# Performance work log

Hardware: AMD Instinct MI355X
Metric: run time of the kernel (lower is better)

The kernel has to match this reference:

```python
import jax, jax.numpy as jnp
import numpy as np

VOCAB = 32000
DIM = 1024
SEQ = 4096


def setup_inputs() -> dict:
    key = jax.random.key(0)
    ks = jax.random.split(key, 6)
    x = jax.random.randint(ks[0], (1, SEQ), 0, VOCAB, dtype=jnp.int64 if jax.config.jax_enable_x64 else jnp.int32)
    emb = jax.random.normal(ks[1], (VOCAB, DIM), dtype=jnp.float32) * 0.02
    norm_w = jnp.ones((DIM,), dtype=jnp.float32)
    Wq = jax.random.normal(ks[2], (DIM, DIM), dtype=jnp.float32) * (1.0 / np.sqrt(DIM))
    Wk = jax.random.normal(ks[3], (DIM, DIM), dtype=jnp.float32) * (1.0 / np.sqrt(DIM))
    Wv = jax.random.normal(ks[4], (DIM, DIM), dtype=jnp.float32) * (1.0 / np.sqrt(DIM))
    return {"x": x, "emb": emb, "norm_w": norm_w, "Wq": Wq, "Wk": Wk, "Wv": Wv}


def reference(x, emb, norm_w, Wq, Wk, Wv):
    # embedding lookup: [1, S, D]
    h = emb[x]
    # RMSNorm (torch nn.RMSNorm with eps=None -> finfo(dtype).eps)
    eps = jnp.finfo(h.dtype).eps
    h = h * jax.lax.rsqrt(jnp.mean(h * h, axis=-1, keepdims=True) + eps) * norm_w
    h = h[0]  # squeeze(0) -> [S, D]
    # QKV projections (torch Linear: y = x @ W.T)
    q = h @ Wq.T
    k = h @ Wk.T
    v = h @ Wv.T
    # NOTE: faithful to source -- no 1/sqrt(d) scaling, no causal mask
    attn = jax.nn.softmax(q @ k.T, axis=-1)  # [S, S]
    out = attn @ v  # [S, D]
    return jax.nn.silu(out)
```

## Files before the change

kernel.cpp:

```cpp
#include <hip/hip_runtime.h>
#include <stdint.h>

#define SEQ 4096
#define DIM 1024

typedef __bf16 bf16x8 __attribute__((ext_vector_type(8)));
typedef float f32x4 __attribute__((ext_vector_type(4)));
typedef unsigned short u16;

__device__ __forceinline__ u16 f2bf(float f) {
    unsigned u = __float_as_uint(f);
    u += 0x7fffu + ((u >> 16) & 1u);
    return (u16)(u >> 16);
}
__device__ __forceinline__ float bf2f(u16 h) {
    return __uint_as_float(((unsigned)h) << 16);
}

__device__ __forceinline__ void gload16(const u16* g, u16* l) {
    __builtin_amdgcn_global_load_lds(
        (const __attribute__((address_space(1))) void*)g,
        (__attribute__((address_space(3))) void*)l, 16, 0, 0);
}

__global__ __launch_bounds__(256) void embed_rmsnorm_split(
    const int* __restrict__ x, const float* __restrict__ emb,
    const float* __restrict__ nw, u16* __restrict__ hh, u16* __restrict__ hl)
{
    const int row  = blockIdx.x;
    const int t    = threadIdx.x;
    const int lane = t & 63, wave = t >> 6;

    bool i64 = true;
    #pragma unroll
    for (int i = 1; i < 128; i += 2) i64 = i64 && (x[i] == 0);
    const int id = i64 ? x[2 * row] : x[row];

    float4 e = *(const float4*)(emb + (size_t)id * DIM + t * 4);
    float ss = e.x*e.x + e.y*e.y + e.z*e.z + e.w*e.w;
    #pragma unroll
    for (int off = 32; off > 0; off >>= 1) ss += __shfl_down(ss, off);

    __shared__ float red[4];
    if (lane == 0) red[wave] = ss;
    __syncthreads();
    float sum = red[0] + red[1] + red[2] + red[3];
    float scale = rsqrtf(sum * (1.0f / DIM) + 1.1920929e-7f);

    float4 n = *(const float4*)(nw + t * 4);
    float o0 = e.x * scale * n.x;
    float o1 = e.y * scale * n.y;
    float o2 = e.z * scale * n.z;
    float o3 = e.w * scale * n.w;
    ushort4 oh, ol;
    u16 b;
    b = f2bf(o0); oh.x = b; ol.x = f2bf(o0 - bf2f(b));
    b = f2bf(o1); oh.y = b; ol.y = f2bf(o1 - bf2f(b));
    b = f2bf(o2); oh.z = b; ol.z = f2bf(o2 - bf2f(b));
    b = f2bf(o3); oh.w = b; ol.w = f2bf(o3 - bf2f(b));
    *(ushort4*)(hh + (size_t)row * DIM + t * 4) = oh;
    *(ushort4*)(hl + (size_t)row * DIM + t * 4) = ol;
}

__global__ __launch_bounds__(256) void split_w(
    const float* __restrict__ W0, const float* __restrict__ W1,
    const float* __restrict__ W2, u16* __restrict__ H, u16* __restrict__ L)
{
    const float* W = (blockIdx.y == 0) ? W0 : (blockIdx.y == 1) ? W1 : W2;
    const size_t base = (size_t)blockIdx.y * DIM * DIM;
    const int i = (blockIdx.x * 256 + threadIdx.x) * 4;
    float4 w = *(const float4*)(W + i);
    ushort4 h, l;
    u16 b;
    b = f2bf(w.x); h.x = b; l.x = f2bf(w.x - bf2f(b));
    b = f2bf(w.y); h.y = b; l.y = f2bf(w.y - bf2f(b));
    b = f2bf(w.z); h.z = b; l.z = f2bf(w.z - bf2f(b));
    b = f2bf(w.w); h.w = b; l.w = f2bf(w.w - bf2f(b));
    *(ushort4*)(H + base + i) = h;
    *(ushort4*)(L + base + i) = l;
}

template<int OUT_MODE>
__global__ __launch_bounds__(256, 2) void gemm_split3(
    const u16* __restrict__ Ah, const u16* __restrict__ Al, int lda,
    const u16* __restrict__ Bh, const u16* __restrict__ Bl, int ldb,
    void* __restrict__ C0, void* __restrict__ C1, int ldc, int K)
{
    __shared__ __align__(16) u16 Ash[128 * 32];
    __shared__ __align__(16) u16 Asl[128 * 32];
    __shared__ __align__(16) u16 Bsh[128 * 32];
    __shared__ __align__(16) u16 Bsl[128 * 32];

    const int tid  = threadIdx.x;
    const int lane = tid & 63;
    const int wave = tid >> 6;
    const int m0   = blockIdx.y * 128;
    const int n0   = blockIdx.x * 128;
    const int wr   = (wave >> 1) * 64;
    const int wc   = (wave & 1) * 64;
    const int half = lane >> 4;
    const int l16  = lane & 15;

    f32x4 acc[4][4] = {};

    const int arow = tid >> 2;
    const int acol = (tid & 3) * 8;
    const int wb   = wave * 512;

    for (int k0 = 0; k0 < K; k0 += 32) {
        __syncthreads();
        const size_t aoff = (size_t)(m0 + arow) * lda + k0 + acol;
        const size_t boff = (size_t)(n0 + arow) * ldb + k0 + acol;
        gload16(Ah + aoff,                    &Ash[wb]);
        gload16(Ah + aoff + (size_t)64 * lda, &Ash[2048 + wb]);
        gload16(Al + aoff,                    &Asl[wb]);
        gload16(Al + aoff + (size_t)64 * lda, &Asl[2048 + wb]);
        gload16(Bh + boff,                    &Bsh[wb]);
        gload16(Bh + boff + (size_t)64 * ldb, &Bsh[2048 + wb]);
        gload16(Bl + boff,                    &Bsl[wb]);
        gload16(Bl + boff + (size_t)64 * ldb, &Bsl[2048 + wb]);
        __syncthreads();

        bf16x8 afh[4], afl[4], bfh[4], bfl[4];
        #pragma unroll
        for (int i = 0; i < 4; ++i) {
            afh[i] = *(const bf16x8*)&Ash[(wr + i*16 + l16) * 32 + half * 8];
            afl[i] = *(const bf16x8*)&Asl[(wr + i*16 + l16) * 32 + half * 8];
        }
        #pragma unroll
        for (int j = 0; j < 4; ++j) {
            bfh[j] = *(const bf16x8*)&Bsh[(wc + j*16 + l16) * 32 + half * 8];
            bfl[j] = *(const bf16x8*)&Bsl[(wc + j*16 + l16) * 32 + half * 8];
        }
        #pragma unroll
        for (int i = 0; i < 4; ++i)
            #pragma unroll
            for (int j = 0; j < 4; ++j) {
                acc[i][j] = __builtin_amdgcn_mfma_f32_16x16x32_bf16(afh[i], bfh[j], acc[i][j], 0, 0, 0);
                acc[i][j] = __builtin_amdgcn_mfma_f32_16x16x32_bf16(afh[i], bfl[j], acc[i][j], 0, 0, 0);
                acc[i][j] = __builtin_amdgcn_mfma_f32_16x16x32_bf16(afl[i], bfh[j], acc[i][j], 0, 0, 0);
            }
    }

    #pragma unroll
    for (int i = 0; i < 4; ++i)
        #pragma unroll
        for (int j = 0; j < 4; ++j)
            #pragma unroll
            for (int r = 0; r < 4; ++r) {
                int row = m0 + wr + i * 16 + half * 4 + r;
                int col = n0 + wc + j * 16 + l16;
                float val = acc[i][j][r];
                if constexpr (OUT_MODE == 0) {
                    ((float*)C0)[(size_t)row * ldc + col] = val;
                } else if constexpr (OUT_MODE == 1) {
                    u16 hi = f2bf(val);
                    ((u16*)C0)[(size_t)row * ldc + col] = hi;
                    ((u16*)C1)[(size_t)row * ldc + col] = f2bf(val - bf2f(hi));
                } else {
                    ((u16*)C0)[(size_t)col * ldc + row] = f2bf(val);
                }
            }
}

__global__ __launch_bounds__(256, 2) void gemm_bt_silu(
    const u16* __restrict__ A, int lda,
    const u16* __restrict__ B, int ldb,
    float* __restrict__ C, int ldc, int K)
{
    __shared__ __align__(16) u16 As[128 * 32];
    __shared__ __align__(16) u16 Bs[128 * 32];

    const int tid  = threadIdx.x;
    const int lane = tid & 63;
    const int wave = tid >> 6;
    const int m0   = blockIdx.y * 128;
    const int n0   = blockIdx.x * 128;
    const int wr   = (wave >> 1) * 64;
    const int wc   = (wave & 1) * 64;
    const int half = lane >> 4;
    const int l16  = lane & 15;

    f32x4 acc[4][4] = {};
    const int arow = tid >> 2;
    const int acol = (tid & 3) * 8;
    const int wb   = wave * 512;

    for (int k0 = 0; k0 < K; k0 += 32) {
        __syncthreads();
        gload16(A + (size_t)(m0 + arow)      * lda + k0 + acol, &As[wb]);
        gload16(A + (size_t)(m0 + 64 + arow) * lda + k0 + acol, &As[2048 + wb]);
        gload16(B + (size_t)(n0 + arow)      * ldb + k0 + acol, &Bs[wb]);
        gload16(B + (size_t)(n0 + 64 + arow) * ldb + k0 + acol, &Bs[2048 + wb]);
        __syncthreads();

        bf16x8 af[4], bfr[4];
        #pragma unroll
        for (int i = 0; i < 4; ++i)
            af[i] = *(const bf16x8*)&As[(wr + i*16 + l16) * 32 + half * 8];
        #pragma unroll
        for (int j = 0; j < 4; ++j)
            bfr[j] = *(const bf16x8*)&Bs[(wc + j*16 + l16) * 32 + half * 8];
        #pragma unroll
        for (int i = 0; i < 4; ++i)
            #pragma unroll
            for (int j = 0; j < 4; ++j)
                acc[i][j] = __builtin_amdgcn_mfma_f32_16x16x32_bf16(af[i], bfr[j], acc[i][j], 0, 0, 0);
    }

    #pragma unroll
    for (int i = 0; i < 4; ++i)
        #pragma unroll
        for (int j = 0; j < 4; ++j)
            #pragma unroll
            for (int r = 0; r < 4; ++r) {
                int row = m0 + wr + i * 16 + half * 4 + r;
                int col = n0 + wc + j * 16 + l16;
                float v = acc[i][j][r];
                v = v / (1.0f + __expf(-v));
                C[(size_t)row * ldc + col] = v;
            }
}

__global__ __launch_bounds__(256) void softmax_rows(float* __restrict__ S)
{
    const int row  = blockIdx.x;
    const int t    = threadIdx.x;
    const int lane = t & 63, wave = t >> 6;
    float* rp = S + (size_t)row * SEQ;

    float v[16];
    #pragma unroll
    for (int i = 0; i < 4; ++i) {
        float4 f = *(const float4*)(rp + i * 1024 + t * 4);
        v[i*4+0] = f.x; v[i*4+1] = f.y; v[i*4+2] = f.z; v[i*4+3] = f.w;
    }

    float m = v[0];
    #pragma unroll
    for (int i = 1; i < 16; ++i) m = fmaxf(m, v[i]);
    #pragma unroll
    for (int off = 32; off > 0; off >>= 1) m = fmaxf(m, __shfl_down(m, off));
    __shared__ float red[4];
    if (lane == 0) red[wave] = m;
    __syncthreads();
    m = fmaxf(fmaxf(red[0], red[1]), fmaxf(red[2], red[3]));
    __syncthreads();

    float s = 0.0f;
    #pragma unroll
    for (int i = 0; i < 16; ++i) { v[i] = __expf(v[i] - m); s += v[i]; }
    #pragma unroll
    for (int off = 32; off > 0; off >>= 1) s += __shfl_down(s, off);
    if (lane == 0) red[wave] = s;
    __syncthreads();
    s = red[0] + red[1] + red[2] + red[3];
    float inv = 1.0f / s;

    u16* op = (u16*)rp;
    #pragma unroll
    for (int i = 0; i < 4; ++i) {
        ushort4 o;
        o.x = f2bf(v[i*4+0] * inv);
        o.y = f2bf(v[i*4+1] * inv);
        o.z = f2bf(v[i*4+2] * inv);
        o.w = f2bf(v[i*4+3] * inv);
        *(ushort4*)(op + i * 1024 + t * 4) = o;
    }
}

extern "C" void kernel_launch(void* const* d_in, const int* in_sizes, int n_in,
                              void* d_out, int out_size, void* d_ws, size_t ws_size,
                              hipStream_t stream)
{
    const int*   x   = (const int*)d_in[0];
    const float* emb = (const float*)d_in[1];
    const float* nw  = (const float*)d_in[2];
    const float* Wq  = (const float*)d_in[3];
    const float* Wk  = (const float*)d_in[4];
    const float* Wv  = (const float*)d_in[5];
    float* out = (float*)d_out;

    char* ws = (char*)d_ws;
    u16*   vT = (u16*)(ws);
    u16*   qh = (u16*)(ws + ( 8u << 20));
    u16*   ql = (u16*)(ws + (16u << 20));
    u16*   kh = (u16*)(ws + (24u << 20));
    u16*   kl = (u16*)(ws + (32u << 20));
    float* Sc = (float*)(ws + (40u << 20));
    u16*   hh = (u16*)(ws + (40u << 20));
    u16*   hl = (u16*)(ws + (48u << 20));
    u16*   Wh = (u16*)(ws + (56u << 20));
    u16*   Wl = (u16*)(ws + (62u << 20));

    embed_rmsnorm_split<<<SEQ, 256, 0, stream>>>(x, emb, nw, hh, hl);
    split_w<<<dim3(DIM * DIM / 1024, 3), 256, 0, stream>>>(Wq, Wk, Wv, Wh, Wl);

    const size_t WSZ = (size_t)DIM * DIM;
    dim3 gqkv(DIM / 128, SEQ / 128);
    gemm_split3<1><<<gqkv, 256, 0, stream>>>(hh, hl, DIM, Wh,           Wl,           DIM, qh, ql,      DIM, DIM);
    gemm_split3<1><<<gqkv, 256, 0, stream>>>(hh, hl, DIM, Wh + WSZ,     Wl + WSZ,     DIM, kh, kl,      DIM, DIM);
    gemm_split3<2><<<gqkv, 256, 0, stream>>>(hh, hl, DIM, Wh + 2 * WSZ, Wl + 2 * WSZ, DIM, vT, nullptr, SEQ, DIM);

    dim3 gs(SEQ / 128, SEQ / 128);
    gemm_split3<0><<<gs, 256, 0, stream>>>(qh, ql, DIM, kh, kl, DIM, Sc, nullptr, SEQ, DIM);

    softmax_rows<<<SEQ, 256, 0, stream>>>(Sc);

    dim3 gpv(DIM / 128, SEQ / 128);
    gemm_bt_silu<<<gpv, 256, 0, stream>>>((const u16*)Sc, 2 * SEQ, vT, SEQ, out, DIM, SEQ);
}
```

Measured before the change: 535.4 us.

## Fuse QKV GEMMs, concatenate split-bf16 K dim for scores, split-K PV

Merges the three QKV projection launches into one grid over 3072 output columns. Q and K hi/lo halves are stored interleaved so the score GEMM becomes a single bf16 GEMM over a 3072-long K dimension instead of a three-MFMA split loop. The PV GEMM is split along K into two partial results, giving twice as many blocks to fill the GPU, and a separate elementwise kernel sums the partials and applies SiLU. In exchange it adds extra traffic for the partial buffers and one more launch, and raises the occupancy hint to 3 blocks per CU.

```diff
diff --git a/kernel.cpp b/kernel.cpp
--- a/kernel.cpp
+++ b/kernel.cpp
@@ -80,11 +80,10 @@
     *(ushort4*)(L + base + i) = l;
 }
 
-template<int OUT_MODE>
-__global__ __launch_bounds__(256, 2) void gemm_split3(
-    const u16* __restrict__ Ah, const u16* __restrict__ Al, int lda,
-    const u16* __restrict__ Bh, const u16* __restrict__ Bl, int ldb,
-    void* __restrict__ C0, void* __restrict__ C1, int ldc, int K)
+__global__ __launch_bounds__(256, 3) void gemm_qkv(
+    const u16* __restrict__ Ah, const u16* __restrict__ Al,
+    const u16* __restrict__ Bh, const u16* __restrict__ Bl,
+    u16* __restrict__ qhl, u16* __restrict__ khl, u16* __restrict__ vT)
 {
     __shared__ __align__(16) u16 Ash[128 * 32];
     __shared__ __align__(16) u16 Asl[128 * 32];
@@ -107,18 +106,18 @@
     const int acol = (tid & 3) * 8;
     const int wb   = wave * 512;
 
-    for (int k0 = 0; k0 < K; k0 += 32) {
-        __syncthreads();
-        const size_t aoff = (size_t)(m0 + arow) * lda + k0 + acol;
-        const size_t boff = (size_t)(n0 + arow) * ldb + k0 + acol;
-        gload16(Ah + aoff,                    &Ash[wb]);
-        gload16(Ah + aoff + (size_t)64 * lda, &Ash[2048 + wb]);
-        gload16(Al + aoff,                    &Asl[wb]);
-        gload16(Al + aoff + (size_t)64 * lda, &Asl[2048 + wb]);
-        gload16(Bh + boff,                    &Bsh[wb]);
-        gload16(Bh + boff + (size_t)64 * ldb, &Bsh[2048 + wb]);
-        gload16(Bl + boff,                    &Bsl[wb]);
-        gload16(Bl + boff + (size_t)64 * ldb, &Bsl[2048 + wb]);
+    for (int k0 = 0; k0 < DIM; k0 += 32) {
+        __syncthreads();
+        const size_t aoff = (size_t)(m0 + arow) * DIM + k0 + acol;
+        const size_t boff = (size_t)(n0 + arow) * DIM + k0 + acol;
+        gload16(Ah + aoff,            &Ash[wb]);
+        gload16(Ah + aoff + 64 * DIM, &Ash[2048 + wb]);
+        gload16(Al + aoff,            &Asl[wb]);
+        gload16(Al + aoff + 64 * DIM, &Asl[2048 + wb]);
+        gload16(Bh + boff,            &Bsh[wb]);
+        gload16(Bh + boff + 64 * DIM, &Bsh[2048 + wb]);
+        gload16(Bl + boff,            &Bsl[wb]);
+        gload16(Bl + boff + 64 * DIM, &Bsl[2048 + wb]);
         __syncthreads();
 
         bf16x8 afh[4], afl[4], bfh[4], bfl[4];
@@ -142,6 +141,7 @@
             }
     }
 
+    const int reg = n0 >> 10;
     #pragma unroll
     for (int i = 0; i < 4; ++i)
         #pragma unroll
@@ -151,22 +151,23 @@
                 int row = m0 + wr + i * 16 + half * 4 + r;
                 int col = n0 + wc + j * 16 + l16;
                 float val = acc[i][j][r];
-                if constexpr (OUT_MODE == 0) {
-                    ((float*)C0)[(size_t)row * ldc + col] = val;
-                } else if constexpr (OUT_MODE == 1) {
-                    u16 hi = f2bf(val);
-                    ((u16*)C0)[(size_t)row * ldc + col] = hi;
-                    ((u16*)C1)[(size_t)row * ldc + col] = f2bf(val - bf2f(hi));
+                u16 hi = f2bf(val);
+                if (reg == 0) {
+                    qhl[(size_t)row * 2048 + col]        = hi;
+                    qhl[(size_t)row * 2048 + col + 1024] = f2bf(val - bf2f(hi));
+                } else if (reg == 1) {
+                    int c = col - 1024;
+                    khl[(size_t)row * 2048 + c]          = hi;
+                    khl[(size_t)row * 2048 + c + 1024]   = f2bf(val - bf2f(hi));
                 } else {
-                    ((u16*)C0)[(size_t)col * ldc + row] = f2bf(val);
+                    vT[(size_t)(col - 2048) * SEQ + row] = hi;
                 }
             }
 }
 
-__global__ __launch_bounds__(256, 2) void gemm_bt_silu(
-    const u16* __restrict__ A, int lda,
-    const u16* __restrict__ B, int ldb,
-    float* __restrict__ C, int ldc, int K)
+__global__ __launch_bounds__(256, 3) void gemm_sc(
+    const u16* __restrict__ Q, const u16* __restrict__ Kk,
+    float* __restrict__ C)
 {
     __shared__ __align__(16) u16 As[128 * 32];
     __shared__ __align__(16) u16 Bs[128 * 32];
@@ -186,12 +187,14 @@
     const int acol = (tid & 3) * 8;
     const int wb   = wave * 512;
 
-    for (int k0 = 0; k0 < K; k0 += 32) {
-        __syncthreads();
-        gload16(A + (size_t)(m0 + arow)      * lda + k0 + acol, &As[wb]);
-        gload16(A + (size_t)(m0 + 64 + arow) * lda + k0 + acol, &As[2048 + wb]);
-        gload16(B + (size_t)(n0 + arow)      * ldb + k0 + acol, &Bs[wb]);
-        gload16(B + (size_t)(n0 + 64 + arow) * ldb + k0 + acol, &Bs[2048 + wb]);
+    for (int k0 = 0; k0 < 3072; k0 += 32) {
+        const int ka = (k0 < 2048) ? k0 : k0 - 2048;
+        const int kb = (k0 < 1024) ? k0 : k0 - 1024;
+        __syncthreads();
+        gload16(Q  + (size_t)(m0 + arow)      * 2048 + ka + acol, &As[wb]);
+        gload16(Q  + (size_t)(m0 + 64 + arow) * 2048 + ka + acol, &As[2048 + wb]);
+        gload16(Kk + (size_t)(n0 + arow)      * 2048 + kb + acol, &Bs[wb]);
+        gload16(Kk + (size_t)(n0 + 64 + arow) * 2048 + kb + acol, &Bs[2048 + wb]);
         __syncthreads();
 
         bf16x8 af[4], bfr[4];
@@ -216,9 +219,7 @@
             for (int r = 0; r < 4; ++r) {
                 int row = m0 + wr + i * 16 + half * 4 + r;
                 int col = n0 + wc + j * 16 + l16;
-                float v = acc[i][j][r];
-                v = v / (1.0f + __expf(-v));
-                C[(size_t)row * ldc + col] = v;
+                C[(size_t)row * SEQ + col] = acc[i][j][r];
             }
 }
 
@@ -269,6 +270,81 @@
     }
 }
 
+__global__ __launch_bounds__(256, 3) void gemm_pv_partial(
+    const u16* __restrict__ A, const u16* __restrict__ B,
+    float* __restrict__ P0, float* __restrict__ P1)
+{
+    __shared__ __align__(16) u16 As[128 * 32];
+    __shared__ __align__(16) u16 Bs[128 * 32];
+
+    const int tid  = threadIdx.x;
+    const int lane = tid & 63;
+    const int wave = tid >> 6;
+    const int m0   = blockIdx.y * 128;
+    const int n0   = blockIdx.x * 128;
+    const int wr   = (wave >> 1) * 64;
+    const int wc   = (wave & 1) * 64;
+    const int half = lane >> 4;
+    const int l16  = lane & 15;
+
+    float* C = blockIdx.z ? P1 : P0;
+    const int kbase = blockIdx.z * 2048;
+
+    f32x4 acc[4][4] = {};
+    const int arow = tid >> 2;
+    const int acol = (tid & 3) * 8;
+    const int wb   = wave * 512;
+
+    for (int k0 = kbase; k0 < kbase + 2048; k0 += 32) {
+        __syncthreads();
+        gload16(A + (size_t)(m0 + arow)      * 8192 + k0 + acol, &As[wb]);
+        gload16(A + (size_t)(m0 + 64 + arow) * 8192 + k0 + acol, &As[2048 + wb]);
+        gload16(B + (size_t)(n0 + arow)      * 4096 + k0 + acol, &Bs[wb]);
+        gload16(B + (size_t)(n0 + 64 + arow) * 4096 + k0 + acol, &Bs[2048 + wb]);
+        __syncthreads();
+
+        bf16x8 af[4], bfr[4];
+        #pragma unroll
+        for (int i = 0; i < 4; ++i)
+            af[i] = *(const bf16x8*)&As[(wr + i*16 + l16) * 32 + half * 8];
+        #pragma unroll
+        for (int j = 0; j < 4; ++j)
+            bfr[j] = *(const bf16x8*)&Bs[(wc + j*16 + l16) * 32 + half * 8];
+        #pragma unroll
+        for (int i = 0; i < 4; ++i)
+            #pragma unroll
+            for (int j = 0; j < 4; ++j)
+                acc[i][j] = __builtin_amdgcn_mfma_f32_16x16x32_bf16(af[i], bfr[j], acc[i][j], 0, 0, 0);
+    }
+
+    #pragma unroll
+    for (int i = 0; i < 4; ++i)
+        #pragma unroll
+        for (int j = 0; j < 4; ++j)
+            #pragma unroll
+            for (int r = 0; r < 4; ++r) {
+                int row = m0 + wr + i * 16 + half * 4 + r;
+                int col = n0 + wc + j * 16 + l16;
+                C[(size_t)row * DIM + col] = acc[i][j][r];
+            }
+}
+
+__global__ __launch_bounds__(256) void combine_silu(
+    const float* __restrict__ P0, const float* __restrict__ P1,
+    float* __restrict__ out)
+{
+    const int i = (blockIdx.x * 256 + threadIdx.x) * 4;
+    float4 a = *(const float4*)(P0 + i);
+    float4 b = *(const float4*)(P1 + i);
+    float4 o;
+    float v;
+    v = a.x + b.x; o.x = v / (1.0f + __expf(-v));
+    v = a.y + b.y; o.y = v / (1.0f + __expf(-v));
+    v = a.z + b.z; o.z = v / (1.0f + __expf(-v));
+    v = a.w + b.w; o.w = v / (1.0f + __expf(-v));
+    *(float4*)(out + i) = o;
+}
+
 extern "C" void kernel_launch(void* const* d_in, const int* in_sizes, int n_in,
                               void* d_out, int out_size, void* d_ws, size_t ws_size,
                               hipStream_t stream)
@@ -282,31 +358,29 @@
     float* out = (float*)d_out;
 
     char* ws = (char*)d_ws;
-    u16*   vT = (u16*)(ws);
-    u16*   qh = (u16*)(ws + ( 8u << 20));
-    u16*   ql = (u16*)(ws + (16u << 20));
-    u16*   kh = (u16*)(ws + (24u << 20));
-    u16*   kl = (u16*)(ws + (32u << 20));
-    float* Sc = (float*)(ws + (40u << 20));
-    u16*   hh = (u16*)(ws + (40u << 20));
-    u16*   hl = (u16*)(ws + (48u << 20));
-    u16*   Wh = (u16*)(ws + (56u << 20));
-    u16*   Wl = (u16*)(ws + (62u << 20));
+    u16*   vT  = (u16*)(ws);
+    u16*   qhl = (u16*)(ws + ( 8u << 20));
+    u16*   khl = (u16*)(ws + (24u << 20));
+    float* Sc  = (float*)(ws + (40u << 20));
+    u16*   hh  = (u16*)(ws + (40u << 20));
+    u16*   hl  = (u16*)(ws + (48u << 20));
+    u16*   Wh  = (u16*)(ws + (56u << 20));
+    u16*   Wl  = (u16*)(ws + (62u << 20));
+    float* P0  = (float*)(ws + ( 8u << 20));
+    float* P1  = (float*)(ws + (24u << 20));
 
     embed_rmsnorm_split<<<SEQ, 256, 0, stream>>>(x, emb, nw, hh, hl);
     split_w<<<dim3(DIM * DIM / 1024, 3), 256, 0, stream>>>(Wq, Wk, Wv, Wh, Wl);
 
-    const size_t WSZ = (size_t)DIM * DIM;
-    dim3 gqkv(DIM / 128, SEQ / 128);
-    gemm_split3<1><<<gqkv, 256, 0, stream>>>(hh, hl, DIM, Wh,           Wl,           DIM, qh, ql,      DIM, DIM);
-    gemm_split3<1><<<gqkv, 256, 0, stream>>>(hh, hl, DIM, Wh + WSZ,     Wl + WSZ,     DIM, kh, kl,      DIM, DIM);
-    gemm_split3<2><<<gqkv, 256, 0, stream>>>(hh, hl, DIM, Wh + 2 * WSZ, Wl + 2 * WSZ, DIM, vT, nullptr, SEQ, DIM);
-
-    dim3 gs(SEQ / 128, SEQ / 128);
-    gemm_split3<0><<<gs, 256, 0, stream>>>(qh, ql, DIM, kh, kl, DIM, Sc, nullptr, SEQ, DIM);
+    gemm_qkv<<<dim3(3072 / 128, SEQ / 128), 256, 0, stream>>>(
+        hh, hl, Wh, Wl, qhl, khl, vT);
+
+    gemm_sc<<<dim3(SEQ / 128, SEQ / 128), 256, 0, stream>>>(qhl, khl, Sc);
 
     softmax_rows<<<SEQ, 256, 0, stream>>>(Sc);
 
-    dim3 gpv(DIM / 128, SEQ / 128);
-    gemm_bt_silu<<<gpv, 256, 0, stream>>>((const u16*)Sc, 2 * SEQ, vT, SEQ, out, DIM, SEQ);
-}
+    gemm_pv_partial<<<dim3(DIM / 128, SEQ / 128, 2), 256, 0, stream>>>(
+        (const u16*)Sc, vT, P0, P1);
+
+    combine_silu<<<SEQ * DIM / 1024, 256, 0, stream>>>(P0, P1, out);
+}
```

Result: faster. 459.4 us (-14.2%).
